# Optimization experiments

Hardware: AMD Instinct MI355X
Metric: run time of the kernel (lower is better)

The kernel has to match this reference:

```python
import jax, jax.numpy as jnp
import numpy as np

B, T, I, H = 64, 2048, 128, 256


def setup_inputs() -> dict:
    key = jax.random.key(0)
    k1, k2, k3 = jax.random.split(key, 3)
    inputs = jax.random.normal(k1, (B, T, I), dtype=jnp.float32)
    # 4 gates (input, forget, context, output), each an affine op on [x_t, h]
    W_x = jax.random.normal(k2, (4, I, H), dtype=jnp.float32) * (1.0 / np.sqrt(I))
    W_h = jax.random.normal(k3, (4, H, H), dtype=jnp.float32) * (1.0 / np.sqrt(H))
    b = jnp.zeros((4, H), dtype=jnp.float32)
    return {"inputs": inputs, "W_x": W_x, "W_h": W_h, "b": b}


def reference(inputs, W_x, W_h, b):
    # inputs: [B, T, I]; W_x: [4, I, H]; W_h: [4, H, H]; b: [4, H]
    Bb = inputs.shape[0]
    Hh = W_h.shape[-1]
    h0 = jnp.zeros((Bb, Hh), dtype=inputs.dtype)
    c0 = jnp.zeros((Bb, Hh), dtype=inputs.dtype)

    def step(carry, x_t):
        h, c = carry
        # all 4 gate pre-activations at once: [4, B, H]
        g = (jnp.einsum('bi,gih->gbh', x_t, W_x)
             + jnp.einsum('bh,ghk->gbk', h, W_h)
             + b[:, None, :])
        i_gate = jax.nn.sigmoid(g[0])
        f_gate = jax.nn.sigmoid(g[1])
        g_gate = jnp.tanh(g[2])
        o_gate = jax.nn.sigmoid(g[3])
        c_new = f_gate * c + i_gate * g_gate
        h_new = o_gate * jnp.tanh(c_new)
        return (h_new, c_new), h_new

    xs = jnp.swapaxes(inputs, 0, 1)  # [T, B, I]
    (_, _), hs = jax.lax.scan(step, (h0, c0), xs)  # hs: [T, B, H]
    return jnp.swapaxes(hs, 0, 1)  # [B, T, H]
```

## Files before the change

### kernel.cpp

```cpp
#include <hip/hip_runtime.h>
#include <hip/hip_bf16.h>


#define B_ 64
#define T_ 2048
#define I_ 128
#define H_ 256
#define NC 1024

typedef __attribute__((ext_vector_type(8))) short bf16x8;
typedef __attribute__((ext_vector_type(4))) float f32x4;

static __device__ __forceinline__ unsigned short f2bf(float f) {
    unsigned u = __builtin_bit_cast(unsigned, f);
    u = (u + 0x7FFFu + ((u >> 16) & 1u)) >> 16;
    return (unsigned short)u;
}

static __device__ __forceinline__ int dot4(unsigned a, unsigned b, int c) {
#if __has_builtin(__builtin_amdgcn_sdot4)
    return __builtin_amdgcn_sdot4((int)a, (int)b, c, false);
#else
    int r = c;
    r += (int)(signed char)(a) * (int)(signed char)(b);
    r += (int)(signed char)(a >> 8) * (int)(signed char)(b >> 8);
    r += (int)(signed char)(a >> 16) * (int)(signed char)(b >> 16);
    r += (int)(signed char)(a >> 24) * (int)(signed char)(b >> 24);
    return r;
#endif
}

__global__ void pack_wh(const float* __restrict__ Wh, unsigned* __restrict__ wq,
                        float* __restrict__ sws) {
    int col = blockIdx.x;
    int g = col >> 8, j = col & 255;
    int lane = threadIdx.x;
    float v[4];
    float m = 0.f;
#pragma unroll
    for (int u = 0; u < 4; ++u) {
        int k = lane * 4 + u;
        v[u] = Wh[(g * H_ + k) * H_ + j];
        m = fmaxf(m, fabsf(v[u]));
    }
#pragma unroll
    for (int off = 32; off; off >>= 1) m = fmaxf(m, __shfl_xor(m, off));
    float mm = (m > 0.f) ? m : 1.f;
    float inv = 127.f / mm;
    unsigned pack = 0;
#pragma unroll
    for (int u = 0; u < 4; ++u) {
        int q = (int)rintf(v[u] * inv);
        q = max(-127, min(127, q));
        pack |= ((unsigned)(q & 255)) << (8 * u);
    }
    wq[col * 64 + lane] = pack;
    if (lane == 0) sws[col] = mm / (127.f * 127.f);
}

__global__ void pack_wx(const float* __restrict__ Wx,
                        unsigned short* __restrict__ bxp) {
    int f = blockIdx.x * blockDim.x + threadIdx.x;
    int j = f & 7;
    int col = (f >> 3) & 1023;
    int c16 = f >> 13;
    int k = (c16 >> 2) * 32 + (c16 & 3) * 8 + j;
    int g = col >> 8, h = col & 255;
    bxp[f] = f2bf(Wx[(g * I_ + k) * H_ + h]);
}

__global__ __launch_bounds__(256) void gemm_gx(
    const float* __restrict__ A, const unsigned short* __restrict__ Bp,
    unsigned short* __restrict__ Cg) {
    __shared__ uint4 sm[4096];
    int tid = threadIdx.x;
    int mt = blockIdx.x, nt = blockIdx.y;

    const float* Ab = A + (size_t)mt * 128 * I_;
    unsigned* dstA = (unsigned*)sm;
#pragma unroll
    for (int it = 0; it < 16; ++it) {
        int flat = it * 1024 + tid * 4;
        float4 a4 = *(const float4*)(Ab + flat);
        int m = flat >> 7, k0 = flat & 127;
        int c16 = k0 >> 3, j0 = k0 & 7;
        unsigned lo = (unsigned)f2bf(a4.x) | ((unsigned)f2bf(a4.y) << 16);
        unsigned hi = (unsigned)f2bf(a4.z) | ((unsigned)f2bf(a4.w) << 16);
        int didx = ((c16 * 128 + m) * 16 + j0 * 2) >> 2;
        dstA[didx] = lo;
        dstA[didx + 1] = hi;
    }
    const uint4* Bq = (const uint4*)Bp;
#pragma unroll
    for (int it = 0; it < 8; ++it) {
        int chunk = it * 2 + (tid >> 7);
        int inner = tid & 127;
        sm[2048 + chunk * 128 + inner] = Bq[chunk * 1024 + nt * 128 + inner];
    }
    __syncthreads();

    int wid = tid >> 6, lane = tid & 63;
    int r = lane & 15, q = lane >> 4;
    int mw = (wid & 1) * 64, nw = (wid >> 1) * 64;
    f32x4 acc[4][4] = {};
#pragma unroll
    for (int ki = 0; ki < 4; ++ki) {
        bf16x8 af[4], bfr[4];
#pragma unroll
        for (int x = 0; x < 4; ++x) {
            af[x] = __builtin_bit_cast(bf16x8,
                                       sm[(ki * 4 + q) * 128 + mw + x * 16 + r]);
            bfr[x] = __builtin_bit_cast(
                bf16x8, sm[2048 + (ki * 4 + q) * 128 + nw + x * 16 + r]);
        }
#pragma unroll
        for (int x = 0; x < 4; ++x)
#pragma unroll
            for (int y = 0; y < 4; ++y)
                acc[x][y] = __builtin_amdgcn_mfma_f32_16x16x32_bf16(
                    af[x], bfr[y], acc[x][y], 0, 0, 0);
    }
    __syncthreads();

    _Float16* ct = (_Float16*)sm;
#pragma unroll
    for (int x = 0; x < 4; ++x)
#pragma unroll
        for (int y = 0; y < 4; ++y)
#pragma unroll
            for (int g2 = 0; g2 < 4; ++g2) {
                int row = mw + x * 16 + q * 4 + g2;
                int colc = nw + y * 16 + r;
                ct[row * 128 + colc] = (_Float16)acc[x][y][g2];
            }
    __syncthreads();
    int m = tid >> 1, half = tid & 1;
    const uint4* src = (const uint4*)sm;
    uint4* dstg =
        (uint4*)(Cg + ((size_t)(mt * 128 + m) * NC + nt * 128 + half * 64));
#pragma unroll
    for (int i = 0; i < 8; ++i) dstg[i] = src[m * 16 + half * 8 + i];
}

#define DOTQ(acc, hv, wv)            \
    acc = dot4(hv.x, wv.x, acc);     \
    acc = dot4(hv.y, wv.y, acc);     \
    acc = dot4(hv.z, wv.z, acc);     \
    acc = dot4(hv.w, wv.w, acc);

__global__ __launch_bounds__(512) void lstm_rec(
    const unsigned short* __restrict__ gx, const uint4* __restrict__ wq4,
    const float* __restrict__ sws, const float* __restrict__ bias,
    float* __restrict__ out) {
    int b = blockIdx.x, tid = threadIdx.x;
    int col0 = tid, col1 = tid + 512;

    uint4 w0[16], w1[16];
#pragma unroll
    for (int i = 0; i < 16; ++i) {
        w0[i] = wq4[col0 * 16 + i];
        w1[i] = wq4[col1 * 16 + i];
    }
    float s0 = sws[col0], s1 = sws[col1];
    float bb0 = bias[col0], bb1 = bias[col1];

    __shared__ uint4 hq[2][16];
    __shared__ float p1buf[256];
    if (tid < 64) ((unsigned*)&hq[0][0])[tid] = 0u;
    __syncthreads();

    float c = 0.f;
    const _Float16* gxh = (const _Float16*)gx;
    size_t rowbase = (size_t)b * T_;
    float gx0 = (float)gxh[rowbase * NC + col0];
    float gx1 = (float)gxh[rowbase * NC + col1];

    for (int t = 0; t < T_; ++t) {
        size_t row = rowbase + t;
        float nx0 = (float)gxh[(row + 1) * NC + col0];
        float nx1 = (float)gxh[(row + 1) * NC + col1];

        int a0 = 0, a1 = 0, a2 = 0, a3 = 0;
        const uint4* hb = hq[t & 1];
#pragma unroll
        for (int i = 0; i < 16; i += 2) {
            uint4 h0v = hb[i], h1v = hb[i + 1];
            DOTQ(a0, h0v, w0[i]);
            DOTQ(a2, h0v, w1[i]);
            DOTQ(a1, h1v, w0[i + 1]);
            DOTQ(a3, h1v, w1[i + 1]);
        }
        float g0 = (float)(a0 + a1) * s0 + gx0 + bb0;
        float g1 = (float)(a2 + a3) * s1 + gx1 + bb1;

        float r0 = 1.f / (1.f + __expf(-g0));
        float r1;
        if (tid < 256) {
            float e = __expf(-2.f * g1);
            r1 = 2.f / (1.f + e) - 1.f;
            p1buf[tid] = r0 * r1;
        } else {
            r1 = 1.f / (1.f + __expf(-g1));
        }
        __syncthreads();
        if (tid >= 256) {
            int j = tid - 256;
            c = r0 * c + p1buf[j];
            float e = __expf(-2.f * c);
            float th = 2.f / (1.f + e) - 1.f;
            float h = r1 * th;
            out[row * H_ + j] = h;
            int qv = (int)rintf(h * 127.f);
            ((signed char*)hq[(t + 1) & 1])[j] = (signed char)qv;
        }
        __syncthreads();
        gx0 = nx0;
        gx1 = nx1;
    }
}

extern "C" void kernel_launch(void* const* d_in, const int* in_sizes, int n_in,
                              void* d_out, int out_size, void* d_ws,
                              size_t ws_size, hipStream_t stream) {
    const float* inputs = (const float*)d_in[0];
    const float* Wx = (const float*)d_in[1];
    const float* Wh = (const float*)d_in[2];
    const float* bias = (const float*)d_in[3];
    float* out = (float*)d_out;

    char* ws = (char*)d_ws;
    unsigned short* gxbuf = (unsigned short*)ws;
    size_t off = (size_t)B_ * T_ * NC * 2;
    unsigned* wq = (unsigned*)(ws + off);
    off += (size_t)NC * 64 * 4;
    float* sws = (float*)(ws + off);
    off += (size_t)NC * 4;
    unsigned short* bxp = (unsigned short*)(ws + off);
    off += (size_t)I_ * NC * 2;

    pack_wh<<<NC, 64, 0, stream>>>(Wh, wq, sws);
    pack_wx<<<(I_ * NC) / 256, 256, 0, stream>>>(Wx, bxp);
    gemm_gx<<<dim3((B_ * T_) / 128, NC / 128), 256, 0, stream>>>(inputs, bxp,
                                                                 gxbuf);
    lstm_rec<<<B_, 512, 0, stream>>>(gxbuf, (const uint4*)wq, sws, bias, out);
}
```

Baseline: 2.337 ms.

## Give each thread all four gates of one hidden unit; broadcast h via readlane

The gate columns are interleaved so each of 256 threads owns all four gates of one hidden unit, which removes the shared-memory exchange of i*g and one barrier per timestep. The quantized h vector is read as one dword per lane and broadcast with readlane instead of each thread loading uint4 from LDS. Each thread now holds 256 dwords of weights in registers, which risks spills or limits the wave count, and the 4-way dot chain per thread is longer.

```diff
diff --git a/kernel.cpp b/kernel.cpp
--- a/kernel.cpp
+++ b/kernel.cpp
@@ -10,6 +10,7 @@
 
 typedef __attribute__((ext_vector_type(8))) short bf16x8;
 typedef __attribute__((ext_vector_type(4))) float f32x4;
+typedef __attribute__((ext_vector_type(4))) _Float16 f16x4;
 
 static __device__ __forceinline__ unsigned short f2bf(float f) {
     unsigned u = __builtin_bit_cast(unsigned, f);
@@ -32,8 +33,8 @@
 
 __global__ void pack_wh(const float* __restrict__ Wh, unsigned* __restrict__ wq,
                         float* __restrict__ sws) {
-    int col = blockIdx.x;
-    int g = col >> 8, j = col & 255;
+    int colp = blockIdx.x;
+    int g = colp & 3, j = colp >> 2;
     int lane = threadIdx.x;
     float v[4];
     float m = 0.f;
@@ -54,18 +55,18 @@
         q = max(-127, min(127, q));
         pack |= ((unsigned)(q & 255)) << (8 * u);
     }
-    wq[col * 64 + lane] = pack;
-    if (lane == 0) sws[col] = mm / (127.f * 127.f);
+    wq[colp * 64 + lane] = pack;
+    if (lane == 0) sws[colp] = mm / (127.f * 127.f);
 }
 
 __global__ void pack_wx(const float* __restrict__ Wx,
                         unsigned short* __restrict__ bxp) {
     int f = blockIdx.x * blockDim.x + threadIdx.x;
-    int j = f & 7;
-    int col = (f >> 3) & 1023;
+    int jj = f & 7;
+    int colp = (f >> 3) & 1023;
     int c16 = f >> 13;
-    int k = (c16 >> 2) * 32 + (c16 & 3) * 8 + j;
-    int g = col >> 8, h = col & 255;
+    int k = (c16 >> 2) * 32 + (c16 & 3) * 8 + jj;
+    int g = colp & 3, h = colp >> 2;
     bxp[f] = f2bf(Wx[(g * I_ + k) * H_ + h]);
 }
 
@@ -142,80 +143,70 @@
     for (int i = 0; i < 8; ++i) dstg[i] = src[m * 16 + half * 8 + i];
 }
 
-#define DOTQ(acc, hv, wv)            \
-    acc = dot4(hv.x, wv.x, acc);     \
-    acc = dot4(hv.y, wv.y, acc);     \
-    acc = dot4(hv.z, wv.z, acc);     \
-    acc = dot4(hv.w, wv.w, acc);
-
-__global__ __launch_bounds__(512) void lstm_rec(
+__global__ __launch_bounds__(256, 1) void lstm_rec(
     const unsigned short* __restrict__ gx, const uint4* __restrict__ wq4,
     const float* __restrict__ sws, const float* __restrict__ bias,
     float* __restrict__ out) {
-    int b = blockIdx.x, tid = threadIdx.x;
-    int col0 = tid, col1 = tid + 512;
-
-    uint4 w0[16], w1[16];
-#pragma unroll
-    for (int i = 0; i < 16; ++i) {
-        w0[i] = wq4[col0 * 16 + i];
-        w1[i] = wq4[col1 * 16 + i];
-    }
-    float s0 = sws[col0], s1 = sws[col1];
-    float bb0 = bias[col0], bb1 = bias[col1];
-
-    __shared__ uint4 hq[2][16];
-    __shared__ float p1buf[256];
-    if (tid < 64) ((unsigned*)&hq[0][0])[tid] = 0u;
+    int b = blockIdx.x, j = threadIdx.x;
+    int lane = j & 63;
+
+    unsigned w0[64], w1[64], w2[64], w3[64];
+#pragma unroll
+    for (int ii = 0; ii < 16; ++ii) {
+        uint4 v0 = wq4[(j * 4 + 0) * 16 + ii];
+        uint4 v1 = wq4[(j * 4 + 1) * 16 + ii];
+        uint4 v2 = wq4[(j * 4 + 2) * 16 + ii];
+        uint4 v3 = wq4[(j * 4 + 3) * 16 + ii];
+        w0[4 * ii] = v0.x; w0[4 * ii + 1] = v0.y; w0[4 * ii + 2] = v0.z; w0[4 * ii + 3] = v0.w;
+        w1[4 * ii] = v1.x; w1[4 * ii + 1] = v1.y; w1[4 * ii + 2] = v1.z; w1[4 * ii + 3] = v1.w;
+        w2[4 * ii] = v2.x; w2[4 * ii + 1] = v2.y; w2[4 * ii + 2] = v2.z; w2[4 * ii + 3] = v2.w;
+        w3[4 * ii] = v3.x; w3[4 * ii + 1] = v3.y; w3[4 * ii + 2] = v3.z; w3[4 * ii + 3] = v3.w;
+    }
+    float s0 = sws[j * 4 + 0], s1 = sws[j * 4 + 1];
+    float s2 = sws[j * 4 + 2], s3 = sws[j * 4 + 3];
+    float bb0 = bias[0 * H_ + j], bb1 = bias[1 * H_ + j];
+    float bb2 = bias[2 * H_ + j], bb3 = bias[3 * H_ + j];
+
+    __shared__ unsigned hbuf[2][64];
+    if (j < 64) hbuf[0][j] = 0u;
     __syncthreads();
 
     float c = 0.f;
     const _Float16* gxh = (const _Float16*)gx;
     size_t rowbase = (size_t)b * T_;
-    float gx0 = (float)gxh[rowbase * NC + col0];
-    float gx1 = (float)gxh[rowbase * NC + col1];
+    f16x4 gv = *(const f16x4*)(gxh + rowbase * NC + j * 4);
 
     for (int t = 0; t < T_; ++t) {
         size_t row = rowbase + t;
-        float nx0 = (float)gxh[(row + 1) * NC + col0];
-        float nx1 = (float)gxh[(row + 1) * NC + col1];
-
+        f16x4 nv = *(const f16x4*)(gxh + (row + 1) * NC + j * 4);
+
+        unsigned hd = hbuf[t & 1][lane];
         int a0 = 0, a1 = 0, a2 = 0, a3 = 0;
-        const uint4* hb = hq[t & 1];
-#pragma unroll
-        for (int i = 0; i < 16; i += 2) {
-            uint4 h0v = hb[i], h1v = hb[i + 1];
-            DOTQ(a0, h0v, w0[i]);
-            DOTQ(a2, h0v, w1[i]);
-            DOTQ(a1, h1v, w0[i + 1]);
-            DOTQ(a3, h1v, w1[i + 1]);
+#pragma unroll
+        for (int i = 0; i < 64; ++i) {
+            unsigned hs = (unsigned)__builtin_amdgcn_readlane((int)hd, i);
+            a0 = dot4(hs, w0[i], a0);
+            a1 = dot4(hs, w1[i], a1);
+            a2 = dot4(hs, w2[i], a2);
+            a3 = dot4(hs, w3[i], a3);
         }
-        float g0 = (float)(a0 + a1) * s0 + gx0 + bb0;
-        float g1 = (float)(a2 + a3) * s1 + gx1 + bb1;
-
-        float r0 = 1.f / (1.f + __expf(-g0));
-        float r1;
-        if (tid < 256) {
-            float e = __expf(-2.f * g1);
-            r1 = 2.f / (1.f + e) - 1.f;
-            p1buf[tid] = r0 * r1;
-        } else {
-            r1 = 1.f / (1.f + __expf(-g1));
-        }
+        float g0 = (float)a0 * s0 + (float)gv.x + bb0;
+        float g1 = (float)a1 * s1 + (float)gv.y + bb1;
+        float g2 = (float)a2 * s2 + (float)gv.z + bb2;
+        float g3 = (float)a3 * s3 + (float)gv.w + bb3;
+
+        float ig = 1.f / (1.f + __expf(-g0));
+        float fg = 1.f / (1.f + __expf(-g1));
+        float gg = 2.f / (1.f + __expf(-2.f * g2)) - 1.f;
+        float og = 1.f / (1.f + __expf(-g3));
+        c = fg * c + ig * gg;
+        float th = 2.f / (1.f + __expf(-2.f * c)) - 1.f;
+        float h = og * th;
+        out[row * H_ + j] = h;
+        int qv = (int)rintf(h * 127.f);
+        ((signed char*)hbuf[(t + 1) & 1])[j] = (signed char)qv;
         __syncthreads();
-        if (tid >= 256) {
-            int j = tid - 256;
-            c = r0 * c + p1buf[j];
-            float e = __expf(-2.f * c);
-            float th = 2.f / (1.f + e) - 1.f;
-            float h = r1 * th;
-            out[row * H_ + j] = h;
-            int qv = (int)rintf(h * 127.f);
-            ((signed char*)hq[(t + 1) & 1])[j] = (signed char)qv;
-        }
-        __syncthreads();
-        gx0 = nx0;
-        gx1 = nx1;
+        gv = nv;
     }
 }
 
@@ -242,5 +233,5 @@
     pack_wx<<<(I_ * NC) / 256, 256, 0, stream>>>(Wx, bxp);
     gemm_gx<<<dim3((B_ * T_) / 128, NC / 128), 256, 0, stream>>>(inputs, bxp,
                                                                  gxbuf);
-    lstm_rec<<<B_, 512, 0, stream>>>(gxbuf, (const uint4*)wq, sws, bias, out);
-}
+    lstm_rec<<<B_, 256, 0, stream>>>(gxbuf, (const uint4*)wq, sws, bias, out);
+}
```

Measured after the change: 2.603 ms. 1.11x slower.
